# Performance work log

Hardware: AMD Instinct MI355X
Metric: run time of the kernel (lower is better)

## Reference

```python
import jax, jax.numpy as jnp
import numpy as np

DIM = 256        # word / relation / entity-type embedding dim
STATEDIM = 256   # agent state dim
VOCAB = 100000
REL_COUNT = 25
T = 128          # sentence length


def _lstm(wvs, Wih, Whh, bih, bhh, reverse):
    # PyTorch LSTMCell gate order: i, f, g, o
    def step(carry, x):
        h, c = carry
        g = x @ Wih.T + bih + h @ Whh.T + bhh
        i, f, gg, o = jnp.split(g, 4)
        c = jax.nn.sigmoid(f) * c + jax.nn.sigmoid(i) * jnp.tanh(gg)
        h = jax.nn.sigmoid(o) * jnp.tanh(c)
        return (h, c), h
    init = (jnp.zeros((DIM,), jnp.float32), jnp.zeros((DIM,), jnp.float32))
    _, hs = jax.lax.scan(step, init, wvs, reverse=reverse)
    return hs


def setup_inputs() -> dict:
    key = jax.random.key(0)
    ks = jax.random.split(key, 32)
    def p(i, shape, scale=0.05):
        return (jax.random.normal(ks[i], shape) * scale).astype(jnp.float32)
    return {
        "text": jax.random.randint(ks[0], (T,), 0, VOCAB, dtype=jnp.int32),
        "wordvector": p(1, (VOCAB, DIM)),
        "relvec": p(2, (REL_COUNT + 1, DIM)),
        "entvec": p(3, (7, DIM)),
        "WihL": p(4, (4 * DIM, DIM)), "WhhL": p(5, (4 * DIM, DIM)),
        "bihL": p(6, (4 * DIM,)), "bhhL": p(7, (4 * DIM,)),
        "WihR": p(8, (4 * DIM, DIM)), "WhhR": p(9, (4 * DIM, DIM)),
        "bihR": p(10, (4 * DIM,)), "bhhR": p(11, (4 * DIM,)),
        "Wt": p(12, (STATEDIM, 3 * DIM + STATEDIM)), "bt": p(13, (STATEDIM,)),
        "Wp": p(14, (REL_COUNT + 1, STATEDIM)), "bp": p(15, (REL_COUNT + 1,)),
        "Wb": p(16, (STATEDIM, 3 * DIM + 2 * STATEDIM)), "bb": p(17, (STATEDIM,)),
        "Wpl": p(18, (REL_COUNT, 7, STATEDIM)), "bpl": p(19, (REL_COUNT, 7)),
        "Wtt": p(20, (STATEDIM, STATEDIM)), "btt": p(21, (STATEDIM,)),
        "Wtb": p(22, (STATEDIM, STATEDIM)), "btb": p(23, (STATEDIM,)),
        "Wbt": p(24, (STATEDIM, STATEDIM)), "bbt": p(25, (STATEDIM,)),
    }


def reference(text, wordvector, relvec, entvec, WihL, WhhL, bihL, bhhL,
              WihR, WhhR, bihR, bhhR, Wt, bt, Wp, bp, Wb, bb, Wpl, bpl,
              Wtt, btt, Wtb, btb, Wbt, bbt):
    # mode = "test_NER": deterministic argmax sampling, dropout disabled.
    wvs = wordvector[text]                               # [T, DIM]
    front = _lstm(wvs, WihL, WhhL, bihL, bhhL, False)    # [T, DIM]
    back = _lstm(wvs, WihR, WhhR, bihR, bhhR, True)      # [T, DIM]
    wordin = jnp.concatenate([front, back], axis=1)      # [T, 2*DIM]

    def bot_rollout(rel_idx, target, memb0):
        Wr, br = Wpl[rel_idx], bpl[rel_idx]              # per-relation head
        def stepb(carry, w):
            memb, ab = carry
            inpb = jnp.concatenate([w, entvec[ab], memb, target])
            outb = jnp.tanh(inpb @ Wb.T + bb)            # dropout off (test)
            probb = jax.nn.softmax(outb @ Wr.T + br)
            ab2 = jnp.argmax(probb).astype(jnp.int32)
            return (outb, ab2), (ab2, probb[ab2])
        (membf, _), (acts, aps) = jax.lax.scan(
            stepb, (memb0, jnp.zeros((), jnp.int32)), wordin)
        return membf, acts, aps

    def top_step(carry, w):
        mem, rel_action = carry
        inp = jnp.concatenate([w, relvec[rel_action], mem])
        outp = jnp.tanh(inp @ Wt.T + bt)                 # dropout off (test)
        prob = jax.nn.softmax(outp @ Wp.T + bp)
        action = jnp.argmax(prob).astype(jnp.int32)
        actprob = prob[action]
        do_ner = action > 0
        rel_next = jnp.where(do_ner, action, rel_action)
        rel_idx = jnp.maximum(action, 1) - 1
        target = outp @ Wtt.T + btt
        memb0 = outp @ Wtb.T + btb
        membf, acts, aps = bot_rollout(rel_idx, target, memb0)
        mem_after = membf @ Wbt.T + bbt
        mem_next = jnp.where(do_ner, mem_after, outp)
        acts = jnp.where(do_ner, acts, 0)
        aps = jnp.where(do_ner, aps, 0.0)
        return (mem_next, rel_next), (action, actprob, acts, aps)

    init = (jnp.zeros((STATEDIM,), jnp.float32), jnp.zeros((), jnp.int32))
    _, (top_actions, top_actprobs, bot_actions, bot_actprobs) = jax.lax.scan(
        top_step, init, wordin)
    # bot rows where no NER sub-rollout fired are zero-filled (orig: empty lists)
    return top_actions, top_actprobs, bot_actions, bot_actprobs
```

## Files before the change

kernel.cpp:

```cpp
#include <hip/hip_runtime.h>
#include <float.h>

constexpr int SEQ  = 128;
constexpr int D    = 256;
constexpr int G    = 1024;
constexpr int NREL = 26;
constexpr int NENT = 7;

typedef float v2f __attribute__((ext_vector_type(2)));

__global__ void k_trans(const float* __restrict__ in, float* __restrict__ out,
                        int rows, int cols, int in_stride, int in_off)
{
    int idx = blockIdx.x * 256 + threadIdx.x;
    if (idx >= rows * cols) return;
    int i = idx % rows;
    int k = idx / rows;
    out[idx] = in[(size_t)i * in_stride + in_off + k];
}

__global__ __launch_bounds__(1024) void k_xg(
    const int* __restrict__ text, const float* __restrict__ wv,
    const float* __restrict__ Wih, const float* __restrict__ bih,
    const float* __restrict__ bhh, float* __restrict__ xg)
{
    int t = blockIdx.x, j = threadIdx.x;
    const float* x  = wv + (size_t)text[t] * D;
    const float* wr = Wih + (size_t)j * D;
    float acc = bih[j] + bhh[j];
    for (int k = 0; k < D; ++k) acc += x[k] * wr[k];
    xg[t * G + j] = acc;
}

__global__ __launch_bounds__(1024) void k_lstm(
    const float* __restrict__ xgF, const float* __restrict__ xgB,
    const float* __restrict__ WHTF, const float* __restrict__ WHTB,
    float* __restrict__ wordin)
{
    int dir = blockIdx.x;
    const float* xg  = dir ? xgB  : xgF;
    const float* WHT = dir ? WHTB : WHTF;
    __shared__ float h[D], c[D], g[G];
    int j = threadIdx.x;
    if (j < D) { h[j] = 0.f; c[j] = 0.f; }
    __syncthreads();
    for (int s = 0; s < SEQ; ++s) {
        int t = dir ? (SEQ - 1 - s) : s;
        float acc = xg[t * G + j];
        for (int k = 0; k < D; ++k) acc += WHT[k * G + j] * h[k];
        g[j] = acc;
        __syncthreads();
        if (j < D) {
            float si = 1.f / (1.f + expf(-g[j]));
            float sf = 1.f / (1.f + expf(-g[D + j]));
            float gg = tanhf(g[2 * D + j]);
            float so = 1.f / (1.f + expf(-g[3 * D + j]));
            float cn = sf * c[j] + si * gg;
            float hn = so * tanhf(cn);
            c[j] = cn; h[j] = hn;
            wordin[t * (2 * D) + dir * D + j] = hn;
        }
        __syncthreads();
    }
}

__global__ __launch_bounds__(256) void k_prep2(
    const float* __restrict__ wordin,
    const float* __restrict__ WTWT, const float* __restrict__ WBWT,
    const float* __restrict__ WTRT, const float* __restrict__ WBET,
    const float* __restrict__ relvec, const float* __restrict__ entvec,
    const float* __restrict__ btv, const float* __restrict__ bbv,
    float* __restrict__ TW, float* __restrict__ BW,
    float* __restrict__ RV, float* __restrict__ EV)
{
    int b = blockIdx.x, i = threadIdx.x;
    if (b < SEQ) {
        const float* w = wordin + b * (2 * D);
        float a1 = btv[i], a2 = bbv[i];
        for (int j = 0; j < 2 * D; ++j) {
            float wv = w[j];
            a1 += wv * WTWT[j * D + i];
            a2 += wv * WBWT[j * D + i];
        }
        TW[b * D + i] = a1;
        BW[b * D + i] = a2;
    } else if (b < SEQ + NREL) {
        int r = b - SEQ;
        const float* x = relvec + r * D;
        float a = 0.f;
        for (int k = 0; k < D; ++k) a += x[k] * WTRT[k * D + i];
        RV[r * D + i] = a;
    } else {
        int e = b - SEQ - NREL;
        const float* x = entvec + e * D;
        float a = 0.f;
        for (int k = 0; k < D; ++k) a += x[k] * WBET[k * D + i];
        EV[e * D + i] = a;
    }
}

__global__ __launch_bounds__(256) void k_m1(
    const float* __restrict__ WBGT, const float* __restrict__ Wtt,
    float* __restrict__ M1T)
{
    int j = blockIdx.x, i = threadIdx.x;
    float a = 0.f;
    for (int k = 0; k < D; ++k) a = fmaf(WBGT[k * D + i], Wtt[k * D + j], a);
    M1T[j * D + i] = a;
}

__global__ __launch_bounds__(256) void k_c1(
    const float* __restrict__ WBGT, const float* __restrict__ btt,
    float* __restrict__ c1)
{
    int i = threadIdx.x;
    float a = 0.f;
    for (int k = 0; k < D; ++k) a = fmaf(WBGT[k * D + i], btt[k], a);
    c1[i] = a;
}

__global__ __launch_bounds__(256) void k_pack7r(
    const float* __restrict__ Wb, float* __restrict__ WREG)
{
    int e = blockIdx.x * 256 + threadIdx.x;
    if (e >= 512 * 60) return;
    int tid = e / 60, q = e % 60;
    int h = tid >> 8, i = tid & 255;
    WREG[e] = Wb[(size_t)i * (5 * D) + 3 * D + h * 128 + q];
}

__global__ __launch_bounds__(256) void k_pack7l(
    const float* __restrict__ Wb, float* __restrict__ WLDS)
{
    int f = blockIdx.x * 256 + threadIdx.x;
    if (f >= 512 * 68) return;
    int f4 = f >> 2, c = f & 3;
    int l = f4 & 63, rest = f4 >> 6;
    int j = rest % 17, wv = rest / 17;
    int tid = wv * 64 + l;
    int h = tid >> 8, i = tid & 255;
    WLDS[f] = Wb[(size_t)i * (5 * D) + 3 * D + h * 128 + 60 + j * 4 + c];
}

__device__ inline float mv_half(const float* __restrict__ Wcol,
                                const float* __restrict__ x)
{
    float a0 = 0.f, a1 = 0.f, a2 = 0.f, a3 = 0.f;
    #pragma unroll
    for (int kk = 0; kk < 128; kk += 4) {
        a0 = fmaf(Wcol[(kk + 0) * D], x[kk + 0], a0);
        a1 = fmaf(Wcol[(kk + 1) * D], x[kk + 1], a1);
        a2 = fmaf(Wcol[(kk + 2) * D], x[kk + 2], a2);
        a3 = fmaf(Wcol[(kk + 3) * D], x[kk + 3], a3);
    }
    return (a0 + a1) + (a2 + a3);
}

template<int W>
__device__ inline void grp_smax(float lv, int n, int lane, int& am, float& pm)
{
    float mx = lv;
    #pragma unroll
    for (int off = W / 2; off; off >>= 1) mx = fmaxf(mx, __shfl_xor(mx, off));
    float e  = (lane < n) ? expf(lv - mx) : 0.f;
    float se = e;
    #pragma unroll
    for (int off = W / 2; off; off >>= 1) se += __shfl_xor(se, off);
    float p  = (lane < n) ? (e / se) : -1.f;
    float q  = p;
    #pragma unroll
    for (int off = W / 2; off; off >>= 1) q = fmaxf(q, __shfl_xor(q, off));
    unsigned long long mask = __ballot(p == q);
    am = __ffsll((long long)mask) - 1;
    pm = q;
}

#define FMA_AB(Wv, Xv)                                                        \
    { float4 xx_ = (Xv);                                                      \
      A0 = __builtin_elementwise_fma((v2f){(Wv).x, (Wv).y},                   \
                                     (v2f){xx_.x, xx_.y}, A0);                \
      A1 = __builtin_elementwise_fma((v2f){(Wv).z, (Wv).w},                   \
                                     (v2f){xx_.z, xx_.w}, A1); }
#define FMA_CD(Wv, Xv)                                                        \
    { float4 xx_ = (Xv);                                                      \
      A2 = __builtin_elementwise_fma((v2f){(Wv).x, (Wv).y},                   \
                                     (v2f){xx_.x, xx_.y}, A2);                \
      A3 = __builtin_elementwise_fma((v2f){(Wv).z, (Wv).w},                   \
                                     (v2f){xx_.z, xx_.w}, A3); }

__global__ __launch_bounds__(512)
void k_main6(
    const float* __restrict__ TW,   const float* __restrict__ BW,
    const float* __restrict__ RV,   const float* __restrict__ EV,
    const float* __restrict__ WTMT, const float* __restrict__ WTBT,
    const float* __restrict__ WBTT, const float* __restrict__ M1T,
    const float* __restrict__ c1v,  const float* __restrict__ WREG,
    const float* __restrict__ WLDS,
    const float* __restrict__ Wp,   const float* __restrict__ bp,
    const float* __restrict__ Wpl,  const float* __restrict__ bpl,
    const float* __restrict__ btb,  const float* __restrict__ bbt,
    float* __restrict__ out)
{
    const int tid  = threadIdx.x;
    const int lane = tid & 63;
    const int wv8  = tid >> 6;
    const int lwv  = wv8 & 3;
    const int h    = tid >> 8;
    const int i    = tid & 255;
    const bool lower = (tid < 256);

    __shared__ __align__(16) float wlds[512 * 68];
    __shared__ __align__(16) float xbuf[2][D];
    __shared__ __align__(16) float psA[2][D], psB[2][D];
    __shared__ __align__(16) float mem[D], outv[D];
    __shared__ __align__(16) float WrSh[NENT * D];
    __shared__ float lpart[4][32];
    __shared__ float brSh[8];

    {
        const float4* g4 = reinterpret_cast<const float4*>(WLDS);
        float4* w4 = reinterpret_cast<float4*>(wlds);
        #pragma unroll
        for (int it = 0; it < 17; ++it) w4[tid + it * 512] = g4[tid + it * 512];
    }

    const float4* wr4 = reinterpret_cast<const float4*>(WREG) + tid * 15;
    float4 wr0 = wr4[0],  wr1 = wr4[1],  wr2 = wr4[2],  wr3 = wr4[3];
    float4 wr4v = wr4[4], wr5 = wr4[5],  wr6 = wr4[6],  wr7 = wr4[7];
    float4 wr8 = wr4[8],  wr9 = wr4[9],  wr10 = wr4[10], wr11 = wr4[11];
    float4 wr12 = wr4[12], wr13 = wr4[13], wr14 = wr4[14];

    float ev0 = 0.f, ev1 = 0.f, ev2 = 0.f, ev3 = 0.f,
          ev4 = 0.f, ev5 = 0.f, ev6 = 0.f;
    if (lower) {
        ev0 = EV[0 * D + i]; ev1 = EV[1 * D + i]; ev2 = EV[2 * D + i];
        ev3 = EV[3 * D + i]; ev4 = EV[4 * D + i]; ev5 = EV[5 * D + i];
        ev6 = EV[6 * D + i];
        mem[i] = 0.f;
    }
    __syncthreads();

    const float4* wbase =
        reinterpret_cast<const float4*>(wlds) + (size_t)wv8 * (17 * 64) + lane;

    const float* WTMh = WTMT + (size_t)h * 128 * D + i;
    const float* WTBh = WTBT + (size_t)h * 128 * D + i;
    const float* WBTh = WBTT + (size_t)h * 128 * D + i;
    const float* M1h  = M1T  + (size_t)h * 128 * D + i;

    int rel = 0;

    for (int t = 0; t < SEQ; ++t) {
        psA[h][i] = mv_half(WTMh, mem + h * 128);
        __syncthreads();
        if (lower) {
            float tot = psA[0][i] + psA[1][i] +
                        TW[t * D + i] + RV[rel * D + i];
            float outp = tanhf(tot);
            outv[i] = outp;
            #pragma unroll 2
            for (int r = 0; r < NREL; ++r) {
                float pp = outp * Wp[r * D + i];
                #pragma unroll
                for (int off = 32; off; off >>= 1) pp += __shfl_xor(pp, off);
                if (lane == 0) lpart[lwv][r] = pp;
            }
        }
        __syncthreads();
        float lv = -FLT_MAX;
        if (lane < NREL)
            lv = lpart[0][lane] + lpart[1][lane] + lpart[2][lane] +
                 lpart[3][lane] + bp[lane];
        int am; float pm;
        grp_smax<32>(lv, NREL, lane, am, pm);
        if (tid == 0) { out[t] = (float)am; out[SEQ + t] = pm; }
        const int action = am;

        if (action > 0) {
            rel = action;
            psA[h][i] = mv_half(WTBh, outv + h * 128);
            psB[h][i] = mv_half(M1h,  outv + h * 128);
            const size_t wbaseW = (size_t)(action - 1) * NENT * D;
            for (int k = tid; k < NENT * D; k += 512) WrSh[k] = Wpl[wbaseW + k];
            if (tid < NENT) brSh[tid] = bpl[(action - 1) * NENT + tid];
            __syncthreads();
            float btm = 0.f, bwc = 0.f;
            if (lower) {
                xbuf[0][i] = psA[0][i] + psA[1][i] + btb[i];
                btm = psB[0][i] + psB[1][i] + c1v[i];
                bwc = BW[i];
            }
            __syncthreads();

            int p = 0, ab = 0;
            for (int s = 0; s < SEQ; ++s) {
                const float4* xb =
                    reinterpret_cast<const float4*>(xbuf[p] + h * 128);
                v2f A0 = {0.f, 0.f}, A1 = {0.f, 0.f},
                    A2 = {0.f, 0.f}, A3 = {0.f, 0.f};
                FMA_AB(wr0,  xb[0])  FMA_CD(wr1,  xb[1])
                FMA_AB(wr2,  xb[2])  FMA_CD(wr3,  xb[3])
                FMA_AB(wr4v, xb[4])  FMA_CD(wr5,  xb[5])
                FMA_AB(wr6,  xb[6])  FMA_CD(wr7,  xb[7])
                FMA_AB(wr8,  xb[8])  FMA_CD(wr9,  xb[9])
                FMA_AB(wr10, xb[10]) FMA_CD(wr11, xb[11])
                FMA_AB(wr12, xb[12]) FMA_CD(wr13, xb[13])
                FMA_AB(wr14, xb[14])
                #pragma unroll
                for (int j = 0; j < 16; j += 2) {
                    float4 wa = wbase[j * 64], wb_ = wbase[(j + 1) * 64];
                    FMA_AB(wa,  xb[15 + j])
                    FMA_CD(wb_, xb[16 + j])
                }
                { float4 wa = wbase[16 * 64]; FMA_AB(wa, xb[31]) }
                v2f AS = (A0 + A1) + (A2 + A3);
                float ms = AS.x + AS.y;
                psA[h][i] = ms;
                __syncthreads();
                if (lower) {
                    float ev = (ab == 0) ? ev0 : (ab == 1) ? ev1 :
                               (ab == 2) ? ev2 : (ab == 3) ? ev3 :
                               (ab == 4) ? ev4 : (ab == 5) ? ev5 : ev6;
                    float tot = ms + psA[1][i] + bwc + ev + btm;
                    float ob = tanhf(tot);
                    xbuf[p ^ 1][i] = ob;
                    #pragma unroll
                    for (int r = 0; r < NENT; ++r) {
                        float pp = ob * WrSh[r * D + i];
                        #pragma unroll
                        for (int off = 32; off; off >>= 1)
                            pp += __shfl_xor(pp, off);
                        if (lane == 0) lpart[lwv][r] = pp;
                    }
                    int sn = (s + 1 < SEQ) ? s + 1 : s;
                    bwc = BW[sn * D + i];
                }
                __syncthreads();
                float lv2 = -FLT_MAX;
                if (lane < NENT)
                    lv2 = lpart[0][lane] + lpart[1][lane] + lpart[2][lane] +
                          lpart[3][lane] + brSh[lane];
                int am2; float pm2;
                grp_smax<8>(lv2, NENT, lane, am2, pm2);
                if (tid == 0) {
                    out[2 * SEQ + t * SEQ + s] = (float)am2;
                    out[2 * SEQ + SEQ * SEQ + t * SEQ + s] = pm2;
                }
                ab = am2;
                p ^= 1;
            }
            psA[h][i] = mv_half(WBTh, xbuf[p] + h * 128);
            __syncthreads();
            if (lower) mem[i] = psA[0][i] + psA[1][i] + bbt[i];
            __syncthreads();
        } else {
            if (lower) mem[i] = outv[i];
            if (tid < SEQ) {
                out[2 * SEQ + t * SEQ + tid] = 0.f;
                out[2 * SEQ + SEQ * SEQ + t * SEQ + tid] = 0.f;
            }
            __syncthreads();
        }
    }
}

extern "C" void kernel_launch(void* const* d_in, const int* in_sizes, int n_in,
                              void* d_out, int out_size, void* d_ws, size_t ws_size,
                              hipStream_t stream)
{
    (void)in_sizes; (void)n_in; (void)out_size; (void)ws_size;
    const int*   text       = (const int*)  d_in[0];
    const float* wordvector = (const float*)d_in[1];
    const float* relvec     = (const float*)d_in[2];
    const float* entvec     = (const float*)d_in[3];
    const float* WihL = (const float*)d_in[4];  const float* WhhL = (const float*)d_in[5];
    const float* bihL = (const float*)d_in[6];  const float* bhhL = (const float*)d_in[7];
    const float* WihR = (const float*)d_in[8];  const float* WhhR = (const float*)d_in[9];
    const float* bihR = (const float*)d_in[10]; const float* bhhR = (const float*)d_in[11];
    const float* Wt   = (const float*)d_in[12]; const float* bt   = (const float*)d_in[13];
    const float* Wp   = (const float*)d_in[14]; const float* bp   = (const float*)d_in[15];
    const float* Wb   = (const float*)d_in[16]; const float* bb   = (const float*)d_in[17];
    const float* Wpl  = (const float*)d_in[18]; const float* bpl  = (const float*)d_in[19];
    const float* Wtt  = (const float*)d_in[20]; const float* btt  = (const float*)d_in[21];
    const float* Wtb  = (const float*)d_in[22]; const float* btb  = (const float*)d_in[23];
    const float* Wbt  = (const float*)d_in[24]; const float* bbt  = (const float*)d_in[25];

    float* ws = (float*)d_ws;
    size_t o = 0;
    auto take = [&](size_t n) { float* p = ws + o; o += n; return p; };
    float* XGF    = take(SEQ * G);
    float* XGB    = take(SEQ * G);
    float* WHLT   = take(D * G);
    float* WHRT   = take(D * G);
    float* WORDIN = take(SEQ * 2 * D);
    float* TW     = take(SEQ * D);
    float* BW     = take(SEQ * D);
    float* RVb    = take(NREL * D);
    float* EVb    = take(NENT * D);
    float* WTWT   = take(2 * D * D);
    float* WTRT   = take(D * D);
    float* WTMT   = take(D * D);
    float* WBWT   = take(2 * D * D);
    float* WBET   = take(D * D);
    float* WBGT   = take(D * D);
    float* WTBT   = take(D * D);
    float* WBTT   = take(D * D);
    float* M1T    = take(D * D);
    float* C1     = take(D);
    float* WREG   = take(512 * 60);
    float* WLDS   = take(512 * 68);

    auto tr = [&](const float* in, float* outp, int rows, int cols, int stride, int off) {
        int n = rows * cols;
        k_trans<<<(n + 255) / 256, 256, 0, stream>>>(in, outp, rows, cols, stride, off);
    };
    tr(WhhL, WHLT, G, D, D, 0);
    tr(WhhR, WHRT, G, D, D, 0);
    tr(Wt,  WTWT, D, 2 * D, G, 0);
    tr(Wt,  WTRT, D, D, G, 512);
    tr(Wt,  WTMT, D, D, G, 768);
    tr(Wb,  WBWT, D, 2 * D, 5 * D, 0);
    tr(Wb,  WBET, D, D, 5 * D, 512);
    tr(Wb,  WBGT, D, D, 5 * D, 1024);
    tr(Wtb, WTBT, D, D, D, 0);
    tr(Wbt, WBTT, D, D, D, 0);

    k_m1<<<D, D, 0, stream>>>(WBGT, Wtt, M1T);
    k_c1<<<1, D, 0, stream>>>(WBGT, btt, C1);
    k_pack7r<<<(512 * 60 + 255) / 256, 256, 0, stream>>>(Wb, WREG);
    k_pack7l<<<(512 * 68 + 255) / 256, 256, 0, stream>>>(Wb, WLDS);

    k_xg<<<SEQ, 1024, 0, stream>>>(text, wordvector, WihL, bihL, bhhL, XGF);
    k_xg<<<SEQ, 1024, 0, stream>>>(text, wordvector, WihR, bihR, bhhR, XGB);
    k_lstm<<<2, 1024, 0, stream>>>(XGF, XGB, WHLT, WHRT, WORDIN);
    k_prep2<<<SEQ + NREL + NENT, 256, 0, stream>>>(WORDIN, WTWT, WBWT, WTRT, WBET,
                                                   relvec, entvec, bt, bb,
                                                   TW, BW, RVb, EVb);
    k_main6<<<1, 512, 0, stream>>>(TW, BW, RVb, EVb, WTMT, WTBT, WBTT, M1T, C1,
                                   WREG, WLDS, Wp, bp, Wpl, bpl, btb, bbt,
                                   (float*)d_out);
}
```

Baseline: 66.11 ms.

## Shrink main kernel to 256 threads with full-length per-thread dot products

Each output element of the serial recurrence is now computed by one thread over all 256 inputs, instead of two threads splitting K=256 into halves and combining partial sums through shared memory. This removes a barrier and a shared-memory reduction from every inner step. The 256-wide weight rows are spread across registers (128 floats), LDS (96 floats) and a global/L2 stream (32 floats) that is reloaded every step, and the logit partials are double-buffered to avoid a race. The cost is half the parallelism, higher register pressure, and extra global loads on the critical path.

```diff
diff --git a/kernel.cpp b/kernel.cpp
--- a/kernel.cpp
+++ b/kernel.cpp
@@ -119,39 +119,44 @@
     c1[i] = a;
 }
 
-__global__ __launch_bounds__(256) void k_pack7r(
+__global__ __launch_bounds__(256) void k_pack8r(
     const float* __restrict__ Wb, float* __restrict__ WREG)
 {
     int e = blockIdx.x * 256 + threadIdx.x;
-    if (e >= 512 * 60) return;
-    int tid = e / 60, q = e % 60;
-    int h = tid >> 8, i = tid & 255;
-    WREG[e] = Wb[(size_t)i * (5 * D) + 3 * D + h * 128 + q];
-}
-
-__global__ __launch_bounds__(256) void k_pack7l(
+    int i = e >> 7, q = e & 127;
+    WREG[e] = Wb[(size_t)i * (5 * D) + 3 * D + q];
+}
+
+__global__ __launch_bounds__(256) void k_pack8l(
     const float* __restrict__ Wb, float* __restrict__ WLDS)
 {
     int f = blockIdx.x * 256 + threadIdx.x;
-    if (f >= 512 * 68) return;
     int f4 = f >> 2, c = f & 3;
     int l = f4 & 63, rest = f4 >> 6;
-    int j = rest % 17, wv = rest / 17;
-    int tid = wv * 64 + l;
-    int h = tid >> 8, i = tid & 255;
-    WLDS[f] = Wb[(size_t)i * (5 * D) + 3 * D + h * 128 + 60 + j * 4 + c];
-}
-
-__device__ inline float mv_half(const float* __restrict__ Wcol,
-                                const float* __restrict__ x)
+    int j = rest % 24, w = rest / 24;
+    WLDS[f] = Wb[(size_t)(w * 64 + l) * (5 * D) + 3 * D + 128 + 4 * j + c];
+}
+
+__global__ __launch_bounds__(256) void k_pack8g(
+    const float* __restrict__ Wb, float* __restrict__ WGL)
+{
+    int f = blockIdx.x * 256 + threadIdx.x;
+    int f4 = f >> 2, c = f & 3;
+    int i = f4 & 255, j = f4 >> 8;
+    WGL[f] = Wb[(size_t)i * (5 * D) + 3 * D + 224 + 4 * j + c];
+}
+
+__device__ inline float mv_full(const float* __restrict__ Wcol,
+                                const float4* __restrict__ x4)
 {
     float a0 = 0.f, a1 = 0.f, a2 = 0.f, a3 = 0.f;
-    #pragma unroll
-    for (int kk = 0; kk < 128; kk += 4) {
-        a0 = fmaf(Wcol[(kk + 0) * D], x[kk + 0], a0);
-        a1 = fmaf(Wcol[(kk + 1) * D], x[kk + 1], a1);
-        a2 = fmaf(Wcol[(kk + 2) * D], x[kk + 2], a2);
-        a3 = fmaf(Wcol[(kk + 3) * D], x[kk + 3], a3);
+    #pragma unroll 8
+    for (int kk = 0; kk < 64; ++kk) {
+        float4 xv = x4[kk];
+        a0 = fmaf(Wcol[(4 * kk + 0) * D], xv.x, a0);
+        a1 = fmaf(Wcol[(4 * kk + 1) * D], xv.y, a1);
+        a2 = fmaf(Wcol[(4 * kk + 2) * D], xv.z, a2);
+        a3 = fmaf(Wcol[(4 * kk + 3) * D], xv.w, a3);
     }
     return (a0 + a1) + (a2 + a3);
 }
@@ -188,14 +193,14 @@
       A3 = __builtin_elementwise_fma((v2f){(Wv).z, (Wv).w},                   \
                                      (v2f){xx_.z, xx_.w}, A3); }
 
-__global__ __launch_bounds__(512)
-void k_main6(
+__global__ __launch_bounds__(256)
+void k_main7(
     const float* __restrict__ TW,   const float* __restrict__ BW,
     const float* __restrict__ RV,   const float* __restrict__ EV,
     const float* __restrict__ WTMT, const float* __restrict__ WTBT,
     const float* __restrict__ WBTT, const float* __restrict__ M1T,
     const float* __restrict__ c1v,  const float* __restrict__ WREG,
-    const float* __restrict__ WLDS,
+    const float* __restrict__ WLDS, const float* __restrict__ WGL,
     const float* __restrict__ Wp,   const float* __restrict__ bp,
     const float* __restrict__ Wpl,  const float* __restrict__ bpl,
     const float* __restrict__ btb,  const float* __restrict__ bbt,
@@ -203,74 +208,63 @@
 {
     const int tid  = threadIdx.x;
     const int lane = tid & 63;
-    const int wv8  = tid >> 6;
-    const int lwv  = wv8 & 3;
-    const int h    = tid >> 8;
-    const int i    = tid & 255;
-    const bool lower = (tid < 256);
-
-    __shared__ __align__(16) float wlds[512 * 68];
+    const int w8   = tid >> 6;
+
+    __shared__ __align__(16) float wlds[256 * 96];
     __shared__ __align__(16) float xbuf[2][D];
-    __shared__ __align__(16) float psA[2][D], psB[2][D];
     __shared__ __align__(16) float mem[D], outv[D];
-    __shared__ __align__(16) float WrSh[NENT * D];
-    __shared__ float lpart[4][32];
+    __shared__ __align__(16) float Esh[NENT * D], WrSh[NENT * D];
+    __shared__ float lpartT[4][32];
+    __shared__ float lpartB[2][4][8];
     __shared__ float brSh[8];
 
     {
         const float4* g4 = reinterpret_cast<const float4*>(WLDS);
         float4* w4 = reinterpret_cast<float4*>(wlds);
         #pragma unroll
-        for (int it = 0; it < 17; ++it) w4[tid + it * 512] = g4[tid + it * 512];
+        for (int it = 0; it < 24; ++it) w4[tid + it * 256] = g4[tid + it * 256];
     }
-
-    const float4* wr4 = reinterpret_cast<const float4*>(WREG) + tid * 15;
-    float4 wr0 = wr4[0],  wr1 = wr4[1],  wr2 = wr4[2],  wr3 = wr4[3];
-    float4 wr4v = wr4[4], wr5 = wr4[5],  wr6 = wr4[6],  wr7 = wr4[7];
-    float4 wr8 = wr4[8],  wr9 = wr4[9],  wr10 = wr4[10], wr11 = wr4[11];
-    float4 wr12 = wr4[12], wr13 = wr4[13], wr14 = wr4[14];
-
-    float ev0 = 0.f, ev1 = 0.f, ev2 = 0.f, ev3 = 0.f,
-          ev4 = 0.f, ev5 = 0.f, ev6 = 0.f;
-    if (lower) {
-        ev0 = EV[0 * D + i]; ev1 = EV[1 * D + i]; ev2 = EV[2 * D + i];
-        ev3 = EV[3 * D + i]; ev4 = EV[4 * D + i]; ev5 = EV[5 * D + i];
-        ev6 = EV[6 * D + i];
-        mem[i] = 0.f;
-    }
+    for (int k = tid; k < NENT * D; k += 256) Esh[k] = EV[k];
+    mem[tid] = 0.f;
+
+    const float4* r4 = reinterpret_cast<const float4*>(WREG) + tid * 32;
+    float4 wr0 = r4[0],   wr1 = r4[1],   wr2 = r4[2],   wr3 = r4[3];
+    float4 wr4 = r4[4],   wr5 = r4[5],   wr6 = r4[6],   wr7 = r4[7];
+    float4 wr8 = r4[8],   wr9 = r4[9],   wr10 = r4[10], wr11 = r4[11];
+    float4 wr12 = r4[12], wr13 = r4[13], wr14 = r4[14], wr15 = r4[15];
+    float4 wr16 = r4[16], wr17 = r4[17], wr18 = r4[18], wr19 = r4[19];
+    float4 wr20 = r4[20], wr21 = r4[21], wr22 = r4[22], wr23 = r4[23];
+    float4 wr24 = r4[24], wr25 = r4[25], wr26 = r4[26], wr27 = r4[27];
+    float4 wr28 = r4[28], wr29 = r4[29], wr30 = r4[30], wr31 = r4[31];
+
     __syncthreads();
 
     const float4* wbase =
-        reinterpret_cast<const float4*>(wlds) + (size_t)wv8 * (17 * 64) + lane;
-
-    const float* WTMh = WTMT + (size_t)h * 128 * D + i;
-    const float* WTBh = WTBT + (size_t)h * 128 * D + i;
-    const float* WBTh = WBTT + (size_t)h * 128 * D + i;
-    const float* M1h  = M1T  + (size_t)h * 128 * D + i;
+        reinterpret_cast<const float4*>(wlds) + (size_t)w8 * (24 * 64) + lane;
+    const float4* gl = reinterpret_cast<const float4*>(WGL) + tid;
+
+    const float* WTMc = WTMT + tid;
+    const float* WTBc = WTBT + tid;
+    const float* WBTc = WBTT + tid;
+    const float* M1c  = M1T  + tid;
 
     int rel = 0;
 
     for (int t = 0; t < SEQ; ++t) {
-        psA[h][i] = mv_half(WTMh, mem + h * 128);
-        __syncthreads();
-        if (lower) {
-            float tot = psA[0][i] + psA[1][i] +
-                        TW[t * D + i] + RV[rel * D + i];
-            float outp = tanhf(tot);
-            outv[i] = outp;
-            #pragma unroll 2
-            for (int r = 0; r < NREL; ++r) {
-                float pp = outp * Wp[r * D + i];
-                #pragma unroll
-                for (int off = 32; off; off >>= 1) pp += __shfl_xor(pp, off);
-                if (lane == 0) lpart[lwv][r] = pp;
-            }
+        float a = mv_full(WTMc, reinterpret_cast<const float4*>(mem));
+        float outp = tanhf(a + TW[t * D + tid] + RV[rel * D + tid]);
+        outv[tid] = outp;
+        for (int r = 0; r < NREL; ++r) {
+            float pp = outp * Wp[r * D + tid];
+            #pragma unroll
+            for (int off = 32; off; off >>= 1) pp += __shfl_xor(pp, off);
+            if (lane == 0) lpartT[w8][r] = pp;
         }
         __syncthreads();
         float lv = -FLT_MAX;
         if (lane < NREL)
-            lv = lpart[0][lane] + lpart[1][lane] + lpart[2][lane] +
-                 lpart[3][lane] + bp[lane];
+            lv = lpartT[0][lane] + lpartT[1][lane] + lpartT[2][lane] +
+                 lpartT[3][lane] + bp[lane];
         int am; float pm;
         grp_smax<32>(lv, NREL, lane, am, pm);
         if (tid == 0) { out[t] = (float)am; out[SEQ + t] = pm; }
@@ -278,68 +272,80 @@
 
         if (action > 0) {
             rel = action;
-            psA[h][i] = mv_half(WTBh, outv + h * 128);
-            psB[h][i] = mv_half(M1h,  outv + h * 128);
-            const size_t wbaseW = (size_t)(action - 1) * NENT * D;
-            for (int k = tid; k < NENT * D; k += 512) WrSh[k] = Wpl[wbaseW + k];
+            float bs = mv_full(WTBc, reinterpret_cast<const float4*>(outv));
+            float cs = mv_full(M1c,  reinterpret_cast<const float4*>(outv));
+            const size_t wb0 = (size_t)(action - 1) * NENT * D;
+            for (int k = tid; k < NENT * D; k += 256) WrSh[k] = Wpl[wb0 + k];
             if (tid < NENT) brSh[tid] = bpl[(action - 1) * NENT + tid];
-            __syncthreads();
-            float btm = 0.f, bwc = 0.f;
-            if (lower) {
-                xbuf[0][i] = psA[0][i] + psA[1][i] + btb[i];
-                btm = psB[0][i] + psB[1][i] + c1v[i];
-                bwc = BW[i];
-            }
+            float btm = cs + c1v[tid];
+            xbuf[0][tid] = bs + btb[tid];
+            float bwc = BW[tid];
             __syncthreads();
 
             int p = 0, ab = 0;
             for (int s = 0; s < SEQ; ++s) {
-                const float4* xb =
-                    reinterpret_cast<const float4*>(xbuf[p] + h * 128);
+                const float4* xb = reinterpret_cast<const float4*>(xbuf[p]);
+                const float4* glv = gl;
+                asm volatile("" : "+v"(glv));
+                float4 g0 = glv[0 * 256], g1 = glv[1 * 256],
+                       g2 = glv[2 * 256], g3 = glv[3 * 256],
+                       g4 = glv[4 * 256], g5 = glv[5 * 256],
+                       g6 = glv[6 * 256], g7 = glv[7 * 256];
+
                 v2f A0 = {0.f, 0.f}, A1 = {0.f, 0.f},
                     A2 = {0.f, 0.f}, A3 = {0.f, 0.f};
                 FMA_AB(wr0,  xb[0])  FMA_CD(wr1,  xb[1])
                 FMA_AB(wr2,  xb[2])  FMA_CD(wr3,  xb[3])
-                FMA_AB(wr4v, xb[4])  FMA_CD(wr5,  xb[5])
+                FMA_AB(wr4,  xb[4])  FMA_CD(wr5,  xb[5])
                 FMA_AB(wr6,  xb[6])  FMA_CD(wr7,  xb[7])
                 FMA_AB(wr8,  xb[8])  FMA_CD(wr9,  xb[9])
                 FMA_AB(wr10, xb[10]) FMA_CD(wr11, xb[11])
                 FMA_AB(wr12, xb[12]) FMA_CD(wr13, xb[13])
-                FMA_AB(wr14, xb[14])
+                FMA_AB(wr14, xb[14]) FMA_CD(wr15, xb[15])
+                __builtin_amdgcn_sched_barrier(0);
+                FMA_AB(wr16, xb[16]) FMA_CD(wr17, xb[17])
+                FMA_AB(wr18, xb[18]) FMA_CD(wr19, xb[19])
+                FMA_AB(wr20, xb[20]) FMA_CD(wr21, xb[21])
+                FMA_AB(wr22, xb[22]) FMA_CD(wr23, xb[23])
+                FMA_AB(wr24, xb[24]) FMA_CD(wr25, xb[25])
+                FMA_AB(wr26, xb[26]) FMA_CD(wr27, xb[27])
+                FMA_AB(wr28, xb[28]) FMA_CD(wr29, xb[29])
+                FMA_AB(wr30, xb[30]) FMA_CD(wr31, xb[31])
+                __builtin_amdgcn_sched_barrier(0);
                 #pragma unroll
-                for (int j = 0; j < 16; j += 2) {
-                    float4 wa = wbase[j * 64], wb_ = wbase[(j + 1) * 64];
-                    FMA_AB(wa,  xb[15 + j])
-                    FMA_CD(wb_, xb[16 + j])
+                for (int j = 0; j < 24; j += 8) {
+                    float4 wa = wbase[(j + 0) * 64], wb_ = wbase[(j + 1) * 64];
+                    float4 wc = wbase[(j + 2) * 64], wd  = wbase[(j + 3) * 64];
+                    float4 we = wbase[(j + 4) * 64], wf  = wbase[(j + 5) * 64];
+                    float4 wg = wbase[(j + 6) * 64], wh  = wbase[(j + 7) * 64];
+                    FMA_AB(wa, xb[32 + j + 0]) FMA_CD(wb_, xb[32 + j + 1])
+                    FMA_AB(wc, xb[32 + j + 2]) FMA_CD(wd,  xb[32 + j + 3])
+                    FMA_AB(we, xb[32 + j + 4]) FMA_CD(wf,  xb[32 + j + 5])
+                    FMA_AB(wg, xb[32 + j + 6]) FMA_CD(wh,  xb[32 + j + 7])
+                    __builtin_amdgcn_sched_barrier(0);
                 }
-                { float4 wa = wbase[16 * 64]; FMA_AB(wa, xb[31]) }
+                FMA_AB(g0, xb[56]) FMA_CD(g1, xb[57])
+                FMA_AB(g2, xb[58]) FMA_CD(g3, xb[59])
+                FMA_AB(g4, xb[60]) FMA_CD(g5, xb[61])
+                FMA_AB(g6, xb[62]) FMA_CD(g7, xb[63])
                 v2f AS = (A0 + A1) + (A2 + A3);
                 float ms = AS.x + AS.y;
-                psA[h][i] = ms;
-                __syncthreads();
-                if (lower) {
-                    float ev = (ab == 0) ? ev0 : (ab == 1) ? ev1 :
-                               (ab == 2) ? ev2 : (ab == 3) ? ev3 :
-                               (ab == 4) ? ev4 : (ab == 5) ? ev5 : ev6;
-                    float tot = ms + psA[1][i] + bwc + ev + btm;
-                    float ob = tanhf(tot);
-                    xbuf[p ^ 1][i] = ob;
+
+                float ob = tanhf(ms + bwc + Esh[ab * D + tid] + btm);
+                xbuf[p ^ 1][tid] = ob;
+                #pragma unroll
+                for (int r = 0; r < NENT; ++r) {
+                    float pp = ob * WrSh[r * D + tid];
                     #pragma unroll
-                    for (int r = 0; r < NENT; ++r) {
-                        float pp = ob * WrSh[r * D + i];
-                        #pragma unroll
-                        for (int off = 32; off; off >>= 1)
-                            pp += __shfl_xor(pp, off);
-                        if (lane == 0) lpart[lwv][r] = pp;
-                    }
-                    int sn = (s + 1 < SEQ) ? s + 1 : s;
-                    bwc = BW[sn * D + i];
+                    for (int off = 32; off; off >>= 1)
+                        pp += __shfl_xor(pp, off);
+                    if (lane == 0) lpartB[p][w8][r] = pp;
                 }
                 __syncthreads();
                 float lv2 = -FLT_MAX;
                 if (lane < NENT)
-                    lv2 = lpart[0][lane] + lpart[1][lane] + lpart[2][lane] +
-                          lpart[3][lane] + brSh[lane];
+                    lv2 = lpartB[p][0][lane] + lpartB[p][1][lane] +
+                          lpartB[p][2][lane] + lpartB[p][3][lane] + brSh[lane];
                 int am2; float pm2;
                 grp_smax<8>(lv2, NENT, lane, am2, pm2);
                 if (tid == 0) {
@@ -347,14 +353,15 @@
                     out[2 * SEQ + SEQ * SEQ + t * SEQ + s] = pm2;
                 }
                 ab = am2;
+                int sn = (s + 1 < SEQ) ? s + 1 : s;
+                bwc = BW[sn * D + tid];
                 p ^= 1;
             }
-            psA[h][i] = mv_half(WBTh, xbuf[p] + h * 128);
-            __syncthreads();
-            if (lower) mem[i] = psA[0][i] + psA[1][i] + bbt[i];
+            float es = mv_full(WBTc, reinterpret_cast<const float4*>(xbuf[p]));
+            mem[tid] = es + bbt[tid];
             __syncthreads();
         } else {
-            if (lower) mem[i] = outv[i];
+            mem[tid] = outp;
             if (tid < SEQ) {
                 out[2 * SEQ + t * SEQ + tid] = 0.f;
                 out[2 * SEQ + SEQ * SEQ + t * SEQ + tid] = 0.f;
@@ -407,8 +414,9 @@
     float* WBTT   = take(D * D);
     float* M1T    = take(D * D);
     float* C1     = take(D);
-    float* WREG   = take(512 * 60);
-    float* WLDS   = take(512 * 68);
+    float* WREG   = take(256 * 128);
+    float* WLDS   = take(256 * 96);
+    float* WGL    = take(256 * 32);
 
     auto tr = [&](const float* in, float* outp, int rows, int cols, int stride, int off) {
         int n = rows * cols;
@@ -427,8 +435,9 @@
 
     k_m1<<<D, D, 0, stream>>>(WBGT, Wtt, M1T);
     k_c1<<<1, D, 0, stream>>>(WBGT, btt, C1);
-    k_pack7r<<<(512 * 60 + 255) / 256, 256, 0, stream>>>(Wb, WREG);
-    k_pack7l<<<(512 * 68 + 255) / 256, 256, 0, stream>>>(Wb, WLDS);
+    k_pack8r<<<128, 256, 0, stream>>>(Wb, WREG);
+    k_pack8l<<<96, 256, 0, stream>>>(Wb, WLDS);
+    k_pack8g<<<32, 256, 0, stream>>>(Wb, WGL);
 
     k_xg<<<SEQ, 1024, 0, stream>>>(text, wordvector, WihL, bihL, bhhL, XGF);
     k_xg<<<SEQ, 1024, 0, stream>>>(text, wordvector, WihR, bihR, bhhR, XGB);
@@ -436,7 +445,7 @@
     k_prep2<<<SEQ + NREL + NENT, 256, 0, stream>>>(WORDIN, WTWT, WBWT, WTRT, WBET,
                                                    relvec, entvec, bt, bb,
                                                    TW, BW, RVb, EVb);
-    k_main6<<<1, 512, 0, stream>>>(TW, BW, RVb, EVb, WTMT, WTBT, WBTT, M1T, C1,
-                                   WREG, WLDS, Wp, bp, Wpl, bpl, btb, bbt,
+    k_main7<<<1, 256, 0, stream>>>(TW, BW, RVb, EVb, WTMT, WTBT, WBTT, M1T, C1,
+                                   WREG, WLDS, WGL, Wp, bp, Wpl, bpl, btb, bbt,
                                    (float*)d_out);
 }
```

Result: no change. 66.93 ms (+1.2%).
